# Kernel optimization log

Measured on AMD Instinct MI355X. Metric: run time of the kernel, lower is better.

## Reference

```python
import jax, jax.numpy as jnp
import numpy as np

SAMPLE_RATE = 16000
FREQ_LOW = 200.0
FREQ_HIGH = 1200.0
# deterministic stand-in for random.uniform(freq_low, freq_high): midpoint
FREQUENCY = 0.5 * (FREQ_LOW + FREQ_HIGH)  # 700 Hz
CUTOFF = FREQUENCY / SAMPLE_RATE          # normalized cutoff, as in cutoff_frequency()
Q = 0.70710678  # standard Butterworth-like quality factor for biquad highpass


def _biquad_highpass_coeffs(cutoff, q):
    # standard audio-EQ-cookbook highpass biquad, cutoff normalized to sample rate
    w0 = 2.0 * np.pi * cutoff
    cw, sw = np.cos(w0), np.sin(w0)
    alpha = sw / (2.0 * q)
    b0 = (1.0 + cw) / 2.0
    b1 = -(1.0 + cw)
    b2 = (1.0 + cw) / 2.0
    a0 = 1.0 + alpha
    a1 = -2.0 * cw
    a2 = 1.0 - alpha
    return (np.float32(b0 / a0), np.float32(b1 / a0), np.float32(b2 / a0),
            np.float32(a1 / a0), np.float32(a2 / a0))


def setup_inputs() -> dict:
    key = jax.random.key(0)
    B, C, T = 128, 2, 65536
    audio = jax.random.normal(key, (B, C, T), dtype=jnp.float32)
    return {"audio": audio}


def reference(audio) -> jnp.ndarray:
    b0, b1, b2, a1, a2 = _biquad_highpass_coeffs(CUTOFF, Q)
    x_t = jnp.moveaxis(audio, -1, 0)  # [T, B, C] for scan over time
    zero = jnp.zeros(x_t.shape[1:], dtype=audio.dtype)

    def step(carry, x):
        x1, x2, y1, y2 = carry
        # IIR biquad difference equation
        y = b0 * x + b1 * x1 + b2 * x2 - a1 * y1 - a2 * y2
        return (x, x1, y, y1), y

    _, y_t = jax.lax.scan(step, (zero, zero, zero, zero), x_t)
    return jnp.moveaxis(y_t, 0, -1)  # [B, C, T]
```

## Files before the change

### kernel.cpp

```cpp
#include <hip/hip_runtime.h>
#include <math.h>


#define T_LEN    65536
#define L_CHUNK  64
#define W_WARM   64
#define TS       32
#define BLK      64
#define ROWS     64
#define BUF_F    (ROWS * TS)
#define BLOCKS_PER_CH 16

#define WAITVM(n) asm volatile("s_waitcnt vmcnt(" #n ")" ::: "memory")

__device__ __forceinline__ void lds_fence() {
    asm volatile("s_waitcnt lgkmcnt(0)" ::: "memory");
}

__device__ __forceinline__ void dma_tile(const float* __restrict__ x,
                                         int base_f, int tile, float* buf)
{
    #pragma unroll
    for (int i = 0; i < 8; ++i) {
        int pos = base_f + i * 512 + tile * TS;
        pos = pos < 0 ? 0 : pos;
        __builtin_amdgcn_global_load_lds(
            (__attribute__((address_space(1))) void*)(void*)(x + pos),
            (__attribute__((address_space(3))) void*)(buf + i * 256),
            16, 0, 0);
    }
}

template <bool WARM>
__device__ __forceinline__ void tile_filter(float* buf, int lane, bool ch0,
    float c_b0, float c_b1, float c_b2, float c_a1, float c_a2,
    float& x1, float& x2, float& y1, float& y2)
{
    float4 r[8];
    #pragma unroll
    for (int g = 0; g < 8; ++g)
        r[g] = *(float4*)&buf[(lane * 8 + ((g + lane) & 7)) * 4];

    if (WARM && ch0) {
        #pragma unroll
        for (int g = 0; g < 8; ++g) r[g] = make_float4(0.f, 0.f, 0.f, 0.f);
    }

    #pragma unroll
    for (int g = 0; g < 8; ++g) {
        float4 v = r[g];
        float yv;
        yv = c_b0*v.x + c_b1*x1 + c_b2*x2 - c_a1*y1 - c_a2*y2;
        x2 = x1; x1 = v.x; y2 = y1; y1 = yv; v.x = yv;
        yv = c_b0*v.y + c_b1*x1 + c_b2*x2 - c_a1*y1 - c_a2*y2;
        x2 = x1; x1 = v.y; y2 = y1; y1 = yv; v.y = yv;
        yv = c_b0*v.z + c_b1*x1 + c_b2*x2 - c_a1*y1 - c_a2*y2;
        x2 = x1; x1 = v.z; y2 = y1; y1 = yv; v.z = yv;
        yv = c_b0*v.w + c_b1*x1 + c_b2*x2 - c_a1*y1 - c_a2*y2;
        x2 = x1; x1 = v.w; y2 = y1; y1 = yv; v.w = yv;
        if (!WARM) r[g] = v;
    }

    if (!WARM) {
        #pragma unroll
        for (int g = 0; g < 8; ++g)
            *(float4*)&buf[(lane * 8 + ((g + lane) & 7)) * 4] = r[g];
    }
}

__global__ __launch_bounds__(BLK, 4)
void hp_biquad_kernel(const float* __restrict__ x, float* __restrict__ y,
                      float c_b0, float c_b1, float c_b2, float c_a1, float c_a2)
{
    __shared__ float bufA[BUF_F];
    __shared__ float bufB[BUF_F];
    const int lane = threadIdx.x;
    const int cg0  = blockIdx.x * ROWS;
    const bool ch0 = ((blockIdx.x & (BLOCKS_PER_CH - 1)) == 0) && (lane == 0);

    const int l0  = lane >> 3;
    const int j0  = ((lane & 7) - l0) & 7;
    const int bsf = (cg0 + l0) * L_CHUNK - W_WARM + j0 * 4;

    float x1 = 0.f, x2 = 0.f, y1 = 0.f, y2 = 0.f;

    dma_tile(x, bsf, 0, bufA);
    dma_tile(x, bsf, 1, bufB);

    WAITVM(8);
    tile_filter<true>(bufA, lane, ch0, c_b0, c_b1, c_b2, c_a1, c_a2, x1, x2, y1, y2);
    lds_fence();
    dma_tile(x, bsf, 2, bufA);

    WAITVM(8);
    tile_filter<true>(bufB, lane, ch0, c_b0, c_b1, c_b2, c_a1, c_a2, x1, x2, y1, y2);
    lds_fence();
    dma_tile(x, bsf, 3, bufB);

    WAITVM(8);
    tile_filter<false>(bufA, lane, ch0, c_b0, c_b1, c_b2, c_a1, c_a2, x1, x2, y1, y2);

    WAITVM(0);
    tile_filter<false>(bufB, lane, ch0, c_b0, c_b1, c_b2, c_a1, c_a2, x1, x2, y1, y2);
    lds_fence();

    const int ybase = cg0 * L_CHUNK + lane * 4;
    #pragma unroll
    for (int p = 0; p < 16; ++p) {
        int q   = lane + p * 64;
        int seg = q >> 4;
        int jj  = q & 15;
        float* b = (jj < 8) ? bufA : bufB;
        int g   = jj & 7;
        float4 v = *(float4*)&b[(seg * 8 + ((g + seg) & 7)) * 4];
        *(float4*)(y + ybase + p * 256) = v;
    }
}

extern "C" void kernel_launch(void* const* d_in, const int* in_sizes, int n_in,
                              void* d_out, int out_size, void* d_ws, size_t ws_size,
                              hipStream_t stream)
{
    const float* x = (const float*)d_in[0];
    float* y = (float*)d_out;

    const double SR = 16000.0, FLO = 200.0, FHI = 1200.0;
    const double freq   = 0.5 * (FLO + FHI);
    const double cutoff = freq / SR;
    const double q      = 0.70710678;
    const double w0 = 2.0 * M_PI * cutoff;
    const double cw = cos(w0), sw = sin(w0);
    const double alpha = sw / (2.0 * q);
    const double b0 = (1.0 + cw) / 2.0;
    const double b1 = -(1.0 + cw);
    const double b2 = (1.0 + cw) / 2.0;
    const double a0 = 1.0 + alpha;
    const double a1 = -2.0 * cw;
    const double a2 = 1.0 - alpha;
    const float fb0 = (float)(b0 / a0), fb1 = (float)(b1 / a0), fb2 = (float)(b2 / a0);
    const float fa1 = (float)(a1 / a0), fa2 = (float)(a2 / a0);

    const int total  = 128 * 2 * T_LEN;
    const int chunks = total / L_CHUNK;
    const int blocks = chunks / ROWS;

    hp_biquad_kernel<<<blocks, BLK, 0, stream>>>(x, y, fb0, fb1, fb2, fa1, fa2);
    (void)in_sizes; (void)n_in; (void)out_size; (void)d_ws; (void)ws_size;
}
```

Baseline: 115.4 us.

## Double chunk length to halve warm-up overhead, using four LDS tile buffers

Each lane now filters a 128-sample chunk instead of 64, keeping the 64-sample warm-up. This halves the fraction of redundant warm-up loads and compute, and halves the block count. To support it, four LDS tile buffers replace two, with deeper prefetch queues and rotated buffer reuse. The cost is twice the LDS per block, which may reduce occupancy, and a longer serial recurrence per thread.

```diff
diff --git a/kernel.cpp b/kernel.cpp
--- a/kernel.cpp
+++ b/kernel.cpp
@@ -3,13 +3,13 @@
 
 
 #define T_LEN    65536
-#define L_CHUNK  64
+#define L_CHUNK  128
 #define W_WARM   64
 #define TS       32
 #define BLK      64
 #define ROWS     64
 #define BUF_F    (ROWS * TS)
-#define BLOCKS_PER_CH 16
+#define BLOCKS_PER_CH 8
 
 #define WAITVM(n) asm volatile("s_waitcnt vmcnt(" #n ")" ::: "memory")
 
@@ -18,11 +18,11 @@
 }
 
 __device__ __forceinline__ void dma_tile(const float* __restrict__ x,
-                                         int base_f, int tile, float* buf)
+                                         int bsf, int tile, float* buf)
 {
     #pragma unroll
     for (int i = 0; i < 8; ++i) {
-        int pos = base_f + i * 512 + tile * TS;
+        int pos = bsf + i * (8 * L_CHUNK) + tile * TS;
         pos = pos < 0 ? 0 : pos;
         __builtin_amdgcn_global_load_lds(
             (__attribute__((address_space(1))) void*)(void*)(x + pos),
@@ -72,8 +72,7 @@
 void hp_biquad_kernel(const float* __restrict__ x, float* __restrict__ y,
                       float c_b0, float c_b1, float c_b2, float c_a1, float c_a2)
 {
-    __shared__ float bufA[BUF_F];
-    __shared__ float bufB[BUF_F];
+    __shared__ float lds4[4 * BUF_F];
     const int lane = threadIdx.x;
     const int cg0  = blockIdx.x * ROWS;
     const bool ch0 = ((blockIdx.x & (BLOCKS_PER_CH - 1)) == 0) && (lane == 0);
@@ -82,37 +81,47 @@
     const int j0  = ((lane & 7) - l0) & 7;
     const int bsf = (cg0 + l0) * L_CHUNK - W_WARM + j0 * 4;
 
+    float* A = lds4;
+    float* B = lds4 + BUF_F;
+    float* C = lds4 + 2 * BUF_F;
+    float* D = lds4 + 3 * BUF_F;
+
     float x1 = 0.f, x2 = 0.f, y1 = 0.f, y2 = 0.f;
 
-    dma_tile(x, bsf, 0, bufA);
-    dma_tile(x, bsf, 1, bufB);
+    dma_tile(x, bsf, 0, A);
+    dma_tile(x, bsf, 1, B);
+    dma_tile(x, bsf, 2, C);
+    dma_tile(x, bsf, 3, D);
 
+    WAITVM(24);
+    tile_filter<true>(A, lane, ch0, c_b0, c_b1, c_b2, c_a1, c_a2, x1, x2, y1, y2);
+    lds_fence();
+    dma_tile(x, bsf, 4, A);
+
+    WAITVM(24);
+    tile_filter<true>(B, lane, ch0, c_b0, c_b1, c_b2, c_a1, c_a2, x1, x2, y1, y2);
+    lds_fence();
+    dma_tile(x, bsf, 5, B);
+
+    WAITVM(24);
+    tile_filter<false>(C, lane, ch0, c_b0, c_b1, c_b2, c_a1, c_a2, x1, x2, y1, y2);
+    WAITVM(16);
+    tile_filter<false>(D, lane, ch0, c_b0, c_b1, c_b2, c_a1, c_a2, x1, x2, y1, y2);
     WAITVM(8);
-    tile_filter<true>(bufA, lane, ch0, c_b0, c_b1, c_b2, c_a1, c_a2, x1, x2, y1, y2);
-    lds_fence();
-    dma_tile(x, bsf, 2, bufA);
-
-    WAITVM(8);
-    tile_filter<true>(bufB, lane, ch0, c_b0, c_b1, c_b2, c_a1, c_a2, x1, x2, y1, y2);
-    lds_fence();
-    dma_tile(x, bsf, 3, bufB);
-
-    WAITVM(8);
-    tile_filter<false>(bufA, lane, ch0, c_b0, c_b1, c_b2, c_a1, c_a2, x1, x2, y1, y2);
-
+    tile_filter<false>(A, lane, ch0, c_b0, c_b1, c_b2, c_a1, c_a2, x1, x2, y1, y2);
     WAITVM(0);
-    tile_filter<false>(bufB, lane, ch0, c_b0, c_b1, c_b2, c_a1, c_a2, x1, x2, y1, y2);
+    tile_filter<false>(B, lane, ch0, c_b0, c_b1, c_b2, c_a1, c_a2, x1, x2, y1, y2);
     lds_fence();
 
     const int ybase = cg0 * L_CHUNK + lane * 4;
     #pragma unroll
-    for (int p = 0; p < 16; ++p) {
+    for (int p = 0; p < 32; ++p) {
         int q   = lane + p * 64;
-        int seg = q >> 4;
-        int jj  = q & 15;
-        float* b = (jj < 8) ? bufA : bufB;
+        int seg = q >> 5;
+        int jj  = q & 31;
         int g   = jj & 7;
-        float4 v = *(float4*)&b[(seg * 8 + ((g + seg) & 7)) * 4];
+        const float* bb = lds4 + (((jj >> 3) + 2) & 3) * BUF_F;
+        float4 v = *(const float4*)&bb[(seg * 8 + ((g + seg) & 7)) * 4];
         *(float4*)(y + ybase + p * 256) = v;
     }
 }
```

Measured after the change: 116.6 us. About the same (+1.0%).
